# Optimization experiments

Hardware: AMD Instinct MI355X
Metric: run time of the kernel (lower is better)

## Reference

```python
import jax, jax.numpy as jnp
import numpy as np

B, H, W, C, N, P = 4, 200, 176, 256, 16384, 65536
EPS = 1e-3  # BatchNorm eps from the torch module


def _bn(x, g, b, axes):
    # training-mode batch norm (batch statistics), matching nn.BatchNorm forward
    m = x.mean(axes, keepdims=True)
    v = x.var(axes, keepdims=True)
    return (x - m) * jax.lax.rsqrt(v + EPS) * g + b


def setup_inputs() -> dict:
    key = jax.random.key(0)
    ks = jax.random.split(key, 16)
    s = 0.05
    d = {}
    d['feats'] = jax.random.normal(ks[0], (B, C, N), jnp.float32)
    d['cb'] = jax.random.randint(ks[1], (P,), 0, B, dtype=jnp.int32)
    d['cy'] = jax.random.randint(ks[2], (P,), 0, H, dtype=jnp.int32)
    d['cx'] = jax.random.randint(ks[3], (P,), 0, W, dtype=jnp.int32)
    # SH head: Linear(256,256,nb)+BN+ReLU, Linear(256,256,nb)+BN+ReLU, Linear(256,9,b)
    d['sh_w1'] = jax.random.normal(ks[4], (C, 256), jnp.float32) * s
    d['sh_g1'] = jnp.ones((256,), jnp.float32); d['sh_b1'] = jnp.zeros((256,), jnp.float32)
    d['sh_w2'] = jax.random.normal(ks[5], (256, 256), jnp.float32) * s
    d['sh_g2'] = jnp.ones((256,), jnp.float32); d['sh_b2'] = jnp.zeros((256,), jnp.float32)
    d['sh_w3'] = jax.random.normal(ks[6], (256, 9), jnp.float32) * s
    d['sh_bias3'] = jnp.zeros((9,), jnp.float32)
    # Gaus head: Linear(256,256,nb)+BN+ReLU, Linear(256,128,nb)+BN+ReLU, Linear(128,1,b)+sigmoid
    d['g_w1'] = jax.random.normal(ks[7], (C, 256), jnp.float32) * s
    d['g_g1'] = jnp.ones((256,), jnp.float32); d['g_b1'] = jnp.zeros((256,), jnp.float32)
    d['g_w2'] = jax.random.normal(ks[8], (256, 128), jnp.float32) * s
    d['g_g2'] = jnp.ones((128,), jnp.float32); d['g_b2'] = jnp.zeros((128,), jnp.float32)
    d['g_w3'] = jax.random.normal(ks[9], (128, 1), jnp.float32) * s
    d['g_bias3'] = jnp.zeros((1,), jnp.float32)
    # conv_out: 3x3 SparseConv2d no-bias + BN + ReLU ; shared_conv: 3x3 SubMConv2d bias + BN + ReLU
    d['cw1'] = jax.random.normal(ks[10], (3, 3, C, C), jnp.float32) * s
    d['c1_g'] = jnp.ones((C,), jnp.float32); d['c1_b'] = jnp.zeros((C,), jnp.float32)
    d['cw2'] = jax.random.normal(ks[11], (3, 3, C, C), jnp.float32) * s
    d['c2_bias'] = jnp.zeros((C,), jnp.float32)
    d['c2_g'] = jnp.ones((C,), jnp.float32); d['c2_b'] = jnp.zeros((C,), jnp.float32)
    return d


def reference(feats, cb, cy, cx, sh_w1, sh_g1, sh_b1, sh_w2, sh_g2, sh_b2, sh_w3, sh_bias3,
              g_w1, g_g1, g_b1, g_w2, g_g2, g_b2, g_w3, g_bias3,
              cw1, c1_g, c1_b, cw2, c2_bias, c2_g, c2_b):
    # [B,C,N] -> [B*N, C] point-wise features
    pw = feats.transpose(0, 2, 1).reshape(-1, C)
    # pool_feature_in_same_voxel: mean of point features sharing a voxel
    vid = cb * (H * W) + cy * W + cx  # [P] linear voxel id over dense BEV grid
    S = B * H * W
    sums = jax.ops.segment_sum(pw, vid, num_segments=S)            # [S, C]
    cnt = jax.ops.segment_sum(jnp.ones((P,), pw.dtype), vid, num_segments=S)
    pooled = sums / jnp.maximum(cnt, 1.0)[:, None]                 # [S, C]
    # SH head
    h = jax.nn.relu(_bn(pooled @ sh_w1, sh_g1, sh_b1, 0))
    h = jax.nn.relu(_bn(h @ sh_w2, sh_g2, sh_b2, 0))
    pred_sh = h @ sh_w3 + sh_bias3                                 # [S, 9]
    # Gaussian head
    g = jax.nn.relu(_bn(pooled @ g_w1, g_g1, g_b1, 0))
    g = jax.nn.relu(_bn(g @ g_w2, g_g2, g_b2, 0))
    pred_gaus = jax.nn.sigmoid(g @ g_w3 + g_bias3)                 # [S, 1]
    # get_sparse_voxel_feature3: SH (DC term) + gaussian modulated voxel features
    sp = pooled * pred_gaus * pred_sh[:, :1]                       # [S, C]
    x = sp.reshape(B, H, W, C)                                      # dense BEV sparse-tensor equivalent
    dn = ('NHWC', 'HWIO', 'NHWC')
    x = jax.lax.conv_general_dilated(x, cw1, (1, 1), 'SAME', dimension_numbers=dn)
    x = jax.nn.relu(_bn(x, c1_g, c1_b, (0, 1, 2)))
    x = jax.lax.conv_general_dilated(x, cw2, (1, 1), 'SAME', dimension_numbers=dn) + c2_bias
    x = jax.nn.relu(_bn(x, c2_g, c2_b, (0, 1, 2)))
    return x
```

## Files before the change

kernel.cpp:

```cpp
#include <hip/hip_runtime.h>
#include <hip/hip_bf16.h>
#include <cstdint>
#include <cstddef>

#define B_DIM 4
#define H_DIM 200
#define W_DIM 176
#define CCH 256
#define NPP 16384
#define NPTS 65536
#define HW 35200
#define S_TOT 140800
#define EPS 1e-3f
#define INV_S (1.0f/140800.0f)

typedef unsigned short ushort_t;
typedef __attribute__((ext_vector_type(8))) short bf16x8;
typedef __attribute__((ext_vector_type(4))) float f32x4;

__device__ __forceinline__ ushort_t f2bf(float f) {
    __hip_bfloat16 h = __float2bfloat16(f);
    return *(ushort_t*)&h;
}
__device__ __forceinline__ float bf2f(ushort_t u) {
    __hip_bfloat16 h = *(__hip_bfloat16*)&u;
    return __bfloat162float(h);
}

__device__ __forceinline__ void async16(const void* g, void* l) {
    __builtin_amdgcn_global_load_lds(
        (const __attribute__((address_space(1))) unsigned int*)g,
        (__attribute__((address_space(3))) unsigned int*)l,
        16, 0, 0);
}

__device__ __forceinline__ void wait_vmcnt0()  { asm volatile("s_waitcnt vmcnt(0)" ::: "memory"); }
__device__ __forceinline__ void wait_vmcnt4()  { asm volatile("s_waitcnt vmcnt(4)" ::: "memory"); }
__device__ __forceinline__ void wait_vmcnt8()  { asm volatile("s_waitcnt vmcnt(8)" ::: "memory"); }
__device__ __forceinline__ void wait_vmcnt10() { asm volatile("s_waitcnt vmcnt(10)" ::: "memory"); }
__device__ __forceinline__ void wait_lgkm0()   { asm volatile("s_waitcnt lgkmcnt(0)" ::: "memory"); }
__device__ __forceinline__ void memfence_compiler() { asm volatile("" ::: "memory"); }

__device__ __forceinline__ bf16x8 bnrelu8(bf16x8 a, const float* __restrict__ sc,
                                          const float* __restrict__ sh) {
    bf16x8 r;
#pragma unroll
    for (int e = 0; e < 8; ++e) {
        float f = bf2f((ushort_t)a[e]);
        r[e] = (short)f2bf(fmaxf(0.f, f * sc[e] + sh[e]));
    }
    return r;
}

__device__ __forceinline__ int xcd_virt(int fid, int n) {
    int q = n >> 3, r = n & 7;
    int xcd = fid & 7, idx = fid >> 3;
    int base = (xcd < r) ? xcd * (q + 1) : r * (q + 1) + (xcd - r) * q;
    return base + idx;
}

__global__ __launch_bounds__(256) void k_transpose(
    const float* __restrict__ feats, ushort_t* __restrict__ FT)
{
    __shared__ float lds[64][65];
    const int b  = blockIdx.z;
    const int c0 = blockIdx.y * 64;
    const int n0 = blockIdx.x * 64;
    const int tid = threadIdx.x;
#pragma unroll
    for (int i = 0; i < 16; ++i) {
        int idx = i * 256 + tid;
        int cr = idx >> 6, nc = idx & 63;
        lds[cr][nc] = feats[((size_t)b * 256 + c0 + cr) * NPP + n0 + nc];
    }
    __syncthreads();
#pragma unroll
    for (int i = 0; i < 16; ++i) {
        int idx = i * 256 + tid;
        int nr = idx >> 6, cc = idx & 63;
        FT[((size_t)b * NPP + n0 + nr) * CCH + c0 + cc] = f2bf(lds[cc][nr]);
    }
}

__global__ __launch_bounds__(256) void k_buildidx(
    const int* __restrict__ cb, const int* __restrict__ cy,
    const int* __restrict__ cx, int* __restrict__ cnt,
    int* __restrict__ pslot, int* __restrict__ vid)
{
    int p = blockIdx.x * 256 + threadIdx.x;
    int v = cb[p] * HW + cy[p] * W_DIM + cx[p];
    vid[p] = v;
    int r = atomicAdd(&cnt[v], 1);
    if (r < 8) pslot[v * 8 + r] = p;
}

__global__ __launch_bounds__(256) void k_poolgather(
    const ushort_t* __restrict__ FT, const int* __restrict__ cnt,
    const int* __restrict__ pslot, const int* __restrict__ vid,
    ushort_t* __restrict__ Pb)
{
    const int wave = threadIdx.x >> 6;
    const int lane = threadIdx.x & 63;
    const int v = blockIdx.x * 4 + wave;
    const int c = cnt[v];
    float a0 = 0.f, a1 = 0.f, a2 = 0.f, a3 = 0.f;
    if (c <= 8) {
        for (int k = 0; k < c; ++k) {
            int p = pslot[v * 8 + k];
            ushort4 r = ((const ushort4*)(FT + (size_t)p * CCH))[lane];
            a0 += bf2f(r.x); a1 += bf2f(r.y); a2 += bf2f(r.z); a3 += bf2f(r.w);
        }
    } else {
        for (int p = 0; p < NPTS; ++p)
            if (vid[p] == v) {
                ushort4 r = ((const ushort4*)(FT + (size_t)p * CCH))[lane];
                a0 += bf2f(r.x); a1 += bf2f(r.y); a2 += bf2f(r.z); a3 += bf2f(r.w);
            }
    }
    float inv = c ? 1.f / (float)c : 0.f;
    ushort4 o;
    o.x = f2bf(a0 * inv); o.y = f2bf(a1 * inv);
    o.z = f2bf(a2 * inv); o.w = f2bf(a3 * inv);
    ((ushort4*)(Pb + (size_t)v * CCH))[lane] = o;
}

__global__ __launch_bounds__(256) void k_gemmma(
    const ushort_t* __restrict__ X, const ushort_t* __restrict__ Wt,
    ushort_t* __restrict__ Y1, ushort_t* __restrict__ Y2, int ldY,
    int bnh, int nblocks,
    float* __restrict__ acc0, float* __restrict__ acc1, int sqoff)
{
    __shared__ ushort_t Asm[2][128 * 64];
    __shared__ ushort_t Bsm[2][128 * 64];
    const int tid  = threadIdx.x;
    const int w    = tid >> 6;
    const int lane = tid & 63;
    const int virt = xcd_virt(blockIdx.x, nblocks);
    const int pi   = virt / bnh;
    const int bn   = (virt % bnh) * 128;
    const int bm   = pi * 128;
    const int wr   = (w >> 1) * 64;
    const int wc   = (w & 1) * 64;

    size_t aoff[4]; size_t boff[4];
#pragma unroll
    for (int j = 0; j < 4; ++j) {
        int row  = 32 * j + 8 * w + (lane >> 3);
        int qlog = (lane & 7) ^ (row & 7);
        aoff[j] = (size_t)(bm + row) * 256 + qlog * 8;
        boff[j] = (size_t)(bn + row) * 256 + qlog * 8;
    }
    const int lo = (w * 8) * 64;

#pragma unroll
    for (int j = 0; j < 4; ++j) async16(X + aoff[j], &Asm[0][(j * 32) * 64 + lo]);
#pragma unroll
    for (int j = 0; j < 4; ++j) async16(Wt + boff[j], &Bsm[0][(j * 32) * 64 + lo]);

    f32x4 acc[4][4] = {};
    for (int kc = 0; kc < 4; ++kc) {
        if (kc < 3) {
#pragma unroll
            for (int j = 0; j < 4; ++j)
                async16(X + aoff[j] + (kc + 1) * 64, &Asm[(kc + 1) & 1][(j * 32) * 64 + lo]);
#pragma unroll
            for (int j = 0; j < 4; ++j)
                async16(Wt + boff[j] + (kc + 1) * 64, &Bsm[(kc + 1) & 1][(j * 32) * 64 + lo]);
            wait_vmcnt8();
        } else {
            wait_vmcnt0();
        }
        __builtin_amdgcn_s_barrier();
        const ushort_t* Ac = Asm[kc & 1];
        const ushort_t* Bc = Bsm[kc & 1];
        __builtin_amdgcn_s_setprio(1);
#pragma unroll
        for (int ks = 0; ks < 2; ++ks) {
            const int q = ks * 4 + (lane >> 4);
            bf16x8 af[4], bfr[4];
#pragma unroll
            for (int i = 0; i < 4; ++i) {
                int ra = wr + i * 16 + (lane & 15);
                af[i] = *(const bf16x8*)&Ac[ra * 64 + ((q ^ (ra & 7)) * 8)];
            }
#pragma unroll
            for (int jn = 0; jn < 4; ++jn) {
                int rn = wc + jn * 16 + (lane & 15);
                bfr[jn] = *(const bf16x8*)&Bc[rn * 64 + ((q ^ (rn & 7)) * 8)];
            }
#pragma unroll
            for (int i = 0; i < 4; ++i)
#pragma unroll
                for (int jn = 0; jn < 4; ++jn)
                    acc[i][jn] = __builtin_amdgcn_mfma_f32_16x16x32_bf16(
                        af[i], bfr[jn], acc[i][jn], 0, 0, 0);
        }
        __builtin_amdgcn_s_setprio(0);
        memfence_compiler();
        __builtin_amdgcn_s_barrier();
    }
    __syncthreads();

    const int crow0 = bm + wr + (lane >> 4) * 4;
    const int ccol0 = bn + wc + (lane & 15);
    float ls[4] = {}, lq[4] = {};
#pragma unroll
    for (int i = 0; i < 4; ++i)
#pragma unroll
        for (int jn = 0; jn < 4; ++jn) {
            int col = ccol0 + jn * 16;
#pragma unroll
            for (int r = 0; r < 4; ++r) {
                float v = acc[i][jn][r];
                ls[jn] += v; lq[jn] += v * v;
                size_t row = (size_t)(crow0 + i * 16 + r);
                if (col < 256) Y1[row * ldY + col] = f2bf(v);
                else           Y2[row * ldY + col - 256] = f2bf(v);
            }
        }
#pragma unroll
    for (int jn = 0; jn < 4; ++jn) {
        ls[jn] += __shfl_xor(ls[jn], 16, 64); ls[jn] += __shfl_xor(ls[jn], 32, 64);
        lq[jn] += __shfl_xor(lq[jn], 16, 64); lq[jn] += __shfl_xor(lq[jn], 32, 64);
    }
    float* red = (float*)&Asm[0][0];
    if (lane < 16) {
#pragma unroll
        for (int jn = 0; jn < 4; ++jn) {
            red[((w * 16 + lane) * 4 + jn) * 2 + 0] = ls[jn];
            red[((w * 16 + lane) * 4 + jn) * 2 + 1] = lq[jn];
        }
    }
    __syncthreads();
    if (tid < 256) {
        int colhalf = tid & 127, isq = tid >> 7;
        int pair = colhalf >> 6, within = colhalf & 63;
        int l16 = within & 15, jn = within >> 4;
        int w0 = pair ? 1 : 0, w1 = pair ? 3 : 2;
        float s = red[((w0 * 16 + l16) * 4 + jn) * 2 + isq]
                + red[((w1 * 16 + l16) * 4 + jn) * 2 + isq];
        int colg = bn + colhalf;
        float* t = (colg < 256) ? acc0 : acc1;
        atomicAdd(&t[(colg & 255) + isq * sqoff], s);
    }
}

__global__ __launch_bounds__(256) void k_gemmma_bn2(
    const ushort_t* __restrict__ X1, const float* __restrict__ a1In,
    const float* __restrict__ g1, const float* __restrict__ b1,
    const ushort_t* __restrict__ W1, ushort_t* __restrict__ Y1o,
    float* __restrict__ a1Out,
    const ushort_t* __restrict__ X2, const float* __restrict__ a2In,
    const float* __restrict__ g2, const float* __restrict__ b2,
    const ushort_t* __restrict__ W2, ushort_t* __restrict__ Y2o,
    float* __restrict__ a2Out)
{
    const bool sh = blockIdx.x < 2200;
    const ushort_t* X   = sh ? X1 : X2;
    const float* accIn  = sh ? a1In : a2In;
    const float* gIn    = sh ? g1 : g2;
    const float* bIn    = sh ? b1 : b2;
    const ushort_t* Wt  = sh ? W1 : W2;
    ushort_t* Y         = sh ? Y1o : Y2o;
    float* accOut       = sh ? a1Out : a2Out;
    const int ldY       = sh ? 256 : 128;
    const int bnh       = sh ? 2 : 1;
    const int fid       = sh ? blockIdx.x : blockIdx.x - 2200;
    const int nblocks   = sh ? 2200 : 1100;
    const int sqoff     = ldY;

    __shared__ ushort_t Asm[2][128 * 64];
    __shared__ ushort_t Bsm[2][128 * 64];
    __shared__ float parS[512];
    const int tid  = threadIdx.x;
    const int w    = tid >> 6;
    const int lane = tid & 63;
    {
        float m = accIn[tid] * INV_S;
        float v = accIn[256 + tid] * INV_S - m * m;
        float sc = gIn[tid] * rsqrtf(v + EPS);
        parS[tid] = sc;
        parS[256 + tid] = bIn[tid] - m * sc;
    }
    __syncthreads();

    const int virt = xcd_virt(fid, nblocks);
    const int pi   = virt / bnh;
    const int bn   = (virt % bnh) * 128;
    const int bm   = pi * 128;
    const int wr   = (w >> 1) * 64;
    const int wc   = (w & 1) * 64;

    const int qlog = (lane & 7) ^ ((8 * w + (lane >> 3)) & 7);
    size_t aoff[4]; size_t boff[4]; int arow[4];
#pragma unroll
    for (int j = 0; j < 4; ++j) {
        int row  = 32 * j + 8 * w + (lane >> 3);
        arow[j] = row;
        aoff[j] = (size_t)(bm + row) * 256 + qlog * 8;
        boff[j] = (size_t)(bn + row) * 256 + qlog * 8;
    }
    const int lo = (w * 8) * 64;
    const int lsub = (lane & 7) * 8;

    bf16x8 ar[2][4];
#pragma unroll
    for (int j = 0; j < 4; ++j) async16(Wt + boff[j], &Bsm[0][(j * 32) * 64 + lo]);
#pragma unroll
    for (int j = 0; j < 4; ++j) ar[0][j] = *(const bf16x8*)(X + aoff[j]);
    {
        const int cb = qlog * 8;
#pragma unroll
        for (int j = 0; j < 4; ++j)
            *(bf16x8*)&Asm[0][arow[j] * 64 + lsub] =
                bnrelu8(ar[0][j], parS + cb, parS + 256 + cb);
    }
    wait_lgkm0();

    f32x4 acc[4][4] = {};
#pragma unroll
    for (int kc = 0; kc < 4; ++kc) {
        if (kc < 3) {
#pragma unroll
            for (int j = 0; j < 4; ++j)
                async16(Wt + boff[j] + (kc + 1) * 64, &Bsm[(kc + 1) & 1][(j * 32) * 64 + lo]);
#pragma unroll
            for (int j = 0; j < 4; ++j)
                ar[(kc + 1) & 1][j] = *(const bf16x8*)(X + aoff[j] + (kc + 1) * 64);
            wait_vmcnt8();
        } else {
            wait_vmcnt0();
        }
        __builtin_amdgcn_s_barrier();
        const ushort_t* Ac = Asm[kc & 1];
        const ushort_t* Bc = Bsm[kc & 1];
        __builtin_amdgcn_s_setprio(1);
#pragma unroll
        for (int ks = 0; ks < 2; ++ks) {
            const int q = ks * 4 + (lane >> 4);
            bf16x8 af[4], bfr[4];
#pragma unroll
            for (int i = 0; i < 4; ++i) {
                int ra = wr + i * 16 + (lane & 15);
                af[i] = *(const bf16x8*)&Ac[ra * 64 + ((q ^ (ra & 7)) * 8)];
            }
#pragma unroll
            for (int jn = 0; jn < 4; ++jn) {
                int rn = wc + jn * 16 + (lane & 15);
                bfr[jn] = *(const bf16x8*)&Bc[rn * 64 + ((q ^ (rn & 7)) * 8)];
            }
#pragma unroll
            for (int i = 0; i < 4; ++i)
#pragma unroll
                for (int jn = 0; jn < 4; ++jn)
                    acc[i][jn] = __builtin_amdgcn_mfma_f32_16x16x32_bf16(
                        af[i], bfr[jn], acc[i][jn], 0, 0, 0);
        }
        __builtin_amdgcn_s_setprio(0);
        if (kc < 3) {
            const int cb = (kc + 1) * 64 + qlog * 8;
#pragma unroll
            for (int j = 0; j < 4; ++j)
                *(bf16x8*)&Asm[(kc + 1) & 1][arow[j] * 64 + lsub] =
                    bnrelu8(ar[(kc + 1) & 1][j], parS + cb, parS + 256 + cb);
            wait_lgkm0();
        }
        memfence_compiler();
        __builtin_amdgcn_s_barrier();
    }
    __syncthreads();

    const int crow0 = bm + wr + (lane >> 4) * 4;
    const int ccol0 = bn + wc + (lane & 15);
    float ls[4] = {}, lq[4] = {};
#pragma unroll
    for (int i = 0; i < 4; ++i)
#pragma unroll
        for (int jn = 0; jn < 4; ++jn) {
            int col = ccol0 + jn * 16;
#pragma unroll
            for (int r = 0; r < 4; ++r) {
                float v = acc[i][jn][r];
                ls[jn] += v; lq[jn] += v * v;
                Y[(size_t)(crow0 + i * 16 + r) * ldY + col] = f2bf(v);
            }
        }
#pragma unroll
    for (int jn = 0; jn < 4; ++jn) {
        ls[jn] += __shfl_xor(ls[jn], 16, 64); ls[jn] += __shfl_xor(ls[jn], 32, 64);
        lq[jn] += __shfl_xor(lq[jn], 16, 64); lq[jn] += __shfl_xor(lq[jn], 32, 64);
    }
    float* red = (float*)&Asm[0][0];
    if (lane < 16) {
#pragma unroll
        for (int jn = 0; jn < 4; ++jn) {
            red[((w * 16 + lane) * 4 + jn) * 2 + 0] = ls[jn];
            red[((w * 16 + lane) * 4 + jn) * 2 + 1] = lq[jn];
        }
    }
    __syncthreads();
    if (tid < 256) {
        int colhalf = tid & 127, isq = tid >> 7;
        int pair = colhalf >> 6, within = colhalf & 63;
        int l16 = within & 15, jn = within >> 4;
        int w0 = pair ? 1 : 0, w1 = pair ? 3 : 2;
        float s = red[((w0 * 16 + l16) * 4 + jn) * 2 + isq]
                + red[((w1 * 16 + l16) * 4 + jn) * 2 + isq];
        atomicAdd(&accOut[(bn + colhalf) + isq * sqoff], s);
    }
}

__global__ __launch_bounds__(256) void k_convmma(
    const ushort_t* __restrict__ X, const ushort_t* __restrict__ Wt,
    ushort_t* __restrict__ Yb, const float* __restrict__ bias,
    const ushort_t* __restrict__ zp, float* __restrict__ accp)
{
    __shared__ ushort_t Asm[2][192 * 64];
    __shared__ ushort_t Bsm[2][128 * 64];
    const int tid  = threadIdx.x;
    const int w    = tid >> 6;
    const int lane = tid & 63;
    const int virt = xcd_virt(blockIdx.x, 2200);
    const int pi   = virt >> 1;
    const int bn   = (virt & 1) * 128;
    const int b    = pi / 275;
    const int rem  = pi % 275;
    const int th   = rem / 11, tw = rem % 11;
    const int y0   = th * 8 - 1, x0 = tw * 16 - 1;
    const int hb   = (w >> 1) * 4;
    const int wc   = (w & 1) * 64;

    const int qlog = (lane & 7) ^ (lane >> 3);
    const ushort_t* asrc[6];
#pragma unroll
    for (int j = 0; j < 6; ++j) {
        int hr = j * 32 + w * 8 + (lane >> 3);
        int ph = hr / 18, pw = hr % 18;
        int y = y0 + ph, x = x0 + pw;
        bool ok = (hr < 180) && ((unsigned)y < (unsigned)H_DIM) &&
                  ((unsigned)x < (unsigned)W_DIM);
        asrc[j] = ok ? X + ((size_t)b * HW + (size_t)y * W_DIM + x) * 256 + qlog * 8
                     : zp + (lane & 7) * 8;
    }
    const ushort_t* bsrc = Wt + (size_t)(bn + w * 8 + (lane >> 3)) * 256 + qlog * 8;
    const int lo = (w * 8) * 64;

#pragma unroll
    for (int j = 0; j < 6; ++j)
        async16(asrc[j], &Asm[0][(j * 32) * 64 + lo]);
#pragma unroll
    for (int j = 0; j < 4; ++j)
        async16(bsrc + (size_t)j * 8192, &Bsm[0][(j * 32) * 64 + lo]);

    f32x4 acc[4][4] = {};
    for (int kc = 0; kc < 4; ++kc) {
        const ushort_t* acur = Asm[kc & 1];
#pragma unroll
        for (int pos = 0; pos < 9; ++pos) {
            const ushort_t* bcur = Bsm[(kc + pos) & 1];
            ushort_t* bnxt = (ushort_t*)Bsm[(kc + pos + 1) & 1];
            if (pos == 0) {
                if (kc < 3) {
#pragma unroll
                    for (int j = 0; j < 6; ++j)
                        async16(asrc[j] + (kc + 1) * 64,
                                &Asm[(kc + 1) & 1][(j * 32) * 64 + lo]);
#pragma unroll
                    for (int j = 0; j < 4; ++j)
                        async16(bsrc + (size_t)65536 + kc * 64 + j * 8192,
                                bnxt + (j * 32) * 64 + lo);
                    wait_vmcnt10();
                } else {
#pragma unroll
                    for (int j = 0; j < 4; ++j)
                        async16(bsrc + (size_t)65536 + kc * 64 + j * 8192,
                                bnxt + (j * 32) * 64 + lo);
                    wait_vmcnt4();
                }
            } else if (pos < 8) {
#pragma unroll
                for (int j = 0; j < 4; ++j)
                    async16(bsrc + (size_t)(pos + 1) * 65536 + kc * 64 + j * 8192,
                            bnxt + (j * 32) * 64 + lo);
                wait_vmcnt4();
            } else if (kc < 3) {
#pragma unroll
                for (int j = 0; j < 4; ++j)
                    async16(bsrc + (size_t)(kc + 1) * 64 + j * 8192,
                            bnxt + (j * 32) * 64 + lo);
                wait_vmcnt4();
            } else {
                wait_vmcnt0();
            }
            __builtin_amdgcn_s_barrier();
            const int dy = pos / 3 - 1, dx = pos % 3 - 1;
            __builtin_amdgcn_s_setprio(1);
#pragma unroll
            for (int ks = 0; ks < 2; ++ks) {
                const int q = ks * 4 + (lane >> 4);
                bf16x8 af[4], bfr[4];
#pragma unroll
                for (int i = 0; i < 4; ++i) {
                    int ri = (hb + i + 1 + dy) * 18 + 1 + dx + (lane & 15);
                    af[i] = *(const bf16x8*)&acur[ri * 64 + ((q ^ (ri & 7)) * 8)];
                }
#pragma unroll
                for (int jn = 0; jn < 4; ++jn) {
                    int rn = wc + jn * 16 + (lane & 15);
                    bfr[jn] = *(const bf16x8*)&bcur[rn * 64 + ((q ^ (rn & 7)) * 8)];
                }
#pragma unroll
                for (int i = 0; i < 4; ++i)
#pragma unroll
                    for (int jn = 0; jn < 4; ++jn)
                        acc[i][jn] = __builtin_amdgcn_mfma_f32_16x16x32_bf16(
                            af[i], bfr[jn], acc[i][jn], 0, 0, 0);
            }
            __builtin_amdgcn_s_setprio(0);
            memfence_compiler();
            __builtin_amdgcn_s_barrier();
        }
    }
    __syncthreads();

    const size_t sbase = (size_t)b * HW + (size_t)(th * 8) * W_DIM + tw * 16;
    const int colb = bn + wc + (lane & 15);
    const int wsub = (lane >> 4) * 4;
    float ls[4] = {}, lq[4] = {};
#pragma unroll
    for (int i = 0; i < 4; ++i) {
        int h = hb + i;
#pragma unroll
        for (int jn = 0; jn < 4; ++jn) {
            int col = colb + jn * 16;
            float bb = bias ? bias[col] : 0.f;
#pragma unroll
            for (int r = 0; r < 4; ++r) {
                size_t s = sbase + (size_t)h * W_DIM + wsub + r;
                float v = acc[i][jn][r] + bb;
                ls[jn] += v; lq[jn] += v * v;
                Yb[s * 256 + col] = f2bf(v);
            }
        }
    }
#pragma unroll
    for (int jn = 0; jn < 4; ++jn) {
        ls[jn] += __shfl_xor(ls[jn], 16, 64); ls[jn] += __shfl_xor(ls[jn], 32, 64);
        lq[jn] += __shfl_xor(lq[jn], 16, 64); lq[jn] += __shfl_xor(lq[jn], 32, 64);
    }
    float* red = (float*)&Asm[0][0];
    if (lane < 16) {
#pragma unroll
        for (int jn = 0; jn < 4; ++jn) {
            red[((w * 16 + lane) * 4 + jn) * 2 + 0] = ls[jn];
            red[((w * 16 + lane) * 4 + jn) * 2 + 1] = lq[jn];
        }
    }
    __syncthreads();
    if (tid < 256) {
        int colhalf = tid & 127, isq = tid >> 7;
        int pair = colhalf >> 6, within = colhalf & 63;
        int l16 = within & 15, jn = within >> 4;
        int w0 = pair ? 1 : 0, w1 = pair ? 3 : 2;
        float s = red[((w0 * 16 + l16) * 4 + jn) * 2 + isq]
                + red[((w1 * 16 + l16) * 4 + jn) * 2 + isq];
        atomicAdd(&accp[(bn + colhalf) + isq * 256], s);
    }
}

__global__ __launch_bounds__(256) void k_convmma_bn(
    const ushort_t* __restrict__ X, const float* __restrict__ par,
    const ushort_t* __restrict__ Wt,
    ushort_t* __restrict__ Yb, const float* __restrict__ bias,
    const ushort_t* __restrict__ zp, float* __restrict__ accp)
{
    __shared__ ushort_t Asm[2][192 * 64];
    __shared__ ushort_t Bsm[2][128 * 64];
    const int tid  = threadIdx.x;
    const int w    = tid >> 6;
    const int lane = tid & 63;
    const int virt = xcd_virt(blockIdx.x, 2200);
    const int pi   = virt >> 1;
    const int bn   = (virt & 1) * 128;
    const int b    = pi / 275;
    const int rem  = pi % 275;
    const int th   = rem / 11, tw = rem % 11;
    const int y0   = th * 8 - 1, x0 = tw * 16 - 1;
    const int hb   = (w >> 1) * 4;
    const int wc   = (w & 1) * 64;

    const int qlog = (lane & 7) ^ (lane >> 3);
    const ushort_t* asrc[6];
    bool okj[6];
    int arow[6];
#pragma unroll
    for (int j = 0; j < 6; ++j) {
        int hr = j * 32 + w * 8 + (lane >> 3);
        arow[j] = hr;
        int ph = hr / 18, pw = hr % 18;
        int y = y0 + ph, x = x0 + pw;
        okj[j] = (hr < 180) && ((unsigned)y < (unsigned)H_DIM) &&
                 ((unsigned)x < (unsigned)W_DIM);
        asrc[j] = okj[j] ? X + ((size_t)b * HW + (size_t)y * W_DIM + x) * 256 + qlog * 8
                         : zp + (lane & 7) * 8;
    }
    const ushort_t* bsrc = Wt + (size_t)(bn + w * 8 + (lane >> 3)) * 256 + qlog * 8;
    const int lo = (w * 8) * 64;
    const int lsub = (lane & 7) * 8;
    const bf16x8 zv = 0;

    bf16x8 areg[6];
#pragma unroll
    for (int j = 0; j < 6; ++j) areg[j] = *(const bf16x8*)(asrc[j]);
#pragma unroll
    for (int j = 0; j < 4; ++j)
        async16(bsrc + (size_t)j * 8192, &Bsm[0][(j * 32) * 64 + lo]);
    {
        const int cb = qlog * 8;
#pragma unroll
        for (int j = 0; j < 6; ++j)
            *(bf16x8*)&Asm[0][arow[j] * 64 + lsub] =
                okj[j] ? bnrelu8(areg[j], par + cb, par + 256 + cb) : zv;
    }
    wait_lgkm0();

    f32x4 acc[4][4] = {};
#pragma unroll
    for (int kc = 0; kc < 4; ++kc) {
        const ushort_t* acur = Asm[kc & 1];
#pragma unroll
        for (int pos = 0; pos < 9; ++pos) {
            const ushort_t* bcur = Bsm[(kc + pos) & 1];
            ushort_t* bnxt = (ushort_t*)Bsm[(kc + pos + 1) & 1];
            if (pos < 8) {
#pragma unroll
                for (int j = 0; j < 4; ++j)
                    async16(bsrc + (size_t)(pos + 1) * 65536 + kc * 64 + j * 8192,
                            bnxt + (j * 32) * 64 + lo);
            } else if (kc < 3) {
#pragma unroll
                for (int j = 0; j < 4; ++j)
                    async16(bsrc + (size_t)(kc + 1) * 64 + j * 8192,
                            bnxt + (j * 32) * 64 + lo);
            }
            if (pos == 5 && kc < 3) {
#pragma unroll
                for (int j = 0; j < 6; ++j)
                    areg[j] = *(const bf16x8*)(asrc[j] + (kc + 1) * 64);
            }
            if (kc == 3 && pos == 8)      wait_vmcnt0();
            else if (pos == 6 && kc < 3)  wait_vmcnt10();
            else                          wait_vmcnt4();
            __builtin_amdgcn_s_barrier();
            const int dy = pos / 3 - 1, dx = pos % 3 - 1;
            __builtin_amdgcn_s_setprio(1);
#pragma unroll
            for (int ks = 0; ks < 2; ++ks) {
                const int q = ks * 4 + (lane >> 4);
                bf16x8 af[4], bfr[4];
#pragma unroll
                for (int i = 0; i < 4; ++i) {
                    int ri = (hb + i + 1 + dy) * 18 + 1 + dx + (lane & 15);
                    af[i] = *(const bf16x8*)&acur[ri * 64 + ((q ^ (ri & 7)) * 8)];
                }
#pragma unroll
                for (int jn = 0; jn < 4; ++jn) {
                    int rn = wc + jn * 16 + (lane & 15);
                    bfr[jn] = *(const bf16x8*)&bcur[rn * 64 + ((q ^ (rn & 7)) * 8)];
                }
#pragma unroll
                for (int i = 0; i < 4; ++i)
#pragma unroll
                    for (int jn = 0; jn < 4; ++jn)
                        acc[i][jn] = __builtin_amdgcn_mfma_f32_16x16x32_bf16(
                            af[i], bfr[jn], acc[i][jn], 0, 0, 0);
            }
            __builtin_amdgcn_s_setprio(0);
            if (pos == 8 && kc < 3) {
                const int cb = (kc + 1) * 64 + qlog * 8;
#pragma unroll
                for (int j = 0; j < 6; ++j)
                    *(bf16x8*)&Asm[(kc + 1) & 1][arow[j] * 64 + lsub] =
                        okj[j] ? bnrelu8(areg[j], par + cb, par + 256 + cb) : zv;
                wait_lgkm0();
            }
            memfence_compiler();
            __builtin_amdgcn_s_barrier();
        }
    }
    __syncthreads();

    const size_t sbase = (size_t)b * HW + (size_t)(th * 8) * W_DIM + tw * 16;
    const int colb = bn + wc + (lane & 15);
    const int wsub = (lane >> 4) * 4;
    float ls[4] = {}, lq[4] = {};
#pragma unroll
    for (int i = 0; i < 4; ++i) {
        int h = hb + i;
#pragma unroll
        for (int jn = 0; jn < 4; ++jn) {
            int col = colb + jn * 16;
            float bb = bias ? bias[col] : 0.f;
#pragma unroll
            for (int r = 0; r < 4; ++r) {
                size_t s = sbase + (size_t)h * W_DIM + wsub + r;
                float v = acc[i][jn][r] + bb;
                ls[jn] += v; lq[jn] += v * v;
                Yb[s * 256 + col] = f2bf(v);
            }
        }
    }
#pragma unroll
    for (int jn = 0; jn < 4; ++jn) {
        ls[jn] += __shfl_xor(ls[jn], 16, 64); ls[jn] += __shfl_xor(ls[jn], 32, 64);
        lq[jn] += __shfl_xor(lq[jn], 16, 64); lq[jn] += __shfl_xor(lq[jn], 32, 64);
    }
    float* red = (float*)&Asm[0][0];
    if (lane < 16) {
#pragma unroll
        for (int jn = 0; jn < 4; ++jn) {
            red[((w * 16 + lane) * 4 + jn) * 2 + 0] = ls[jn];
            red[((w * 16 + lane) * 4 + jn) * 2 + 1] = lq[jn];
        }
    }
    __syncthreads();
    if (tid < 256) {
        int colhalf = tid & 127, isq = tid >> 7;
        int pair = colhalf >> 6, within = colhalf & 63;
        int l16 = within & 15, jn = within >> 4;
        int w0 = pair ? 1 : 0, w1 = pair ? 3 : 2;
        float s = red[((w0 * 16 + l16) * 4 + jn) * 2 + isq]
                + red[((w1 * 16 + l16) * 4 + jn) * 2 + isq];
        atomicAdd(&accp[(bn + colhalf) + isq * 256], s);
    }
}

__global__ __launch_bounds__(256) void k_castw(
    const float* __restrict__ Wc, ushort_t* __restrict__ Wt, int CO)
{
    int pc = blockIdx.x;
    int co = pc % CO, pos = pc / CO, ci = threadIdx.x;
    Wt[(size_t)pc * 256 + ci] = f2bf(Wc[((size_t)pos * 256 + ci) * CO + co]);
}

__global__ void k_bnparams(const float* __restrict__ acc,
                           const float* __restrict__ g,
                           const float* __restrict__ b,
                           float* __restrict__ par, int ncols)
{
    int c = threadIdx.x;
    if (c >= ncols) return;
    float m = acc[c] * INV_S;
    float v = acc[ncols + c] * INV_S - m * m;
    float sc = g[c] * rsqrtf(v + EPS);
    par[c] = sc;
    par[ncols + c] = b[c] - m * sc;
}

__global__ __launch_bounds__(256) void k_headfin(
    const ushort_t* __restrict__ B2, const ushort_t* __restrict__ B3,
    const float* __restrict__ acc1, const float* __restrict__ shg2,
    const float* __restrict__ shb2,
    const float* __restrict__ acc3, const float* __restrict__ gg2,
    const float* __restrict__ gb2,
    const float* __restrict__ shw3, const float* __restrict__ shb3,
    const float* __restrict__ gw3, const float* __restrict__ gb3,
    const ushort_t* __restrict__ Pb, ushort_t* __restrict__ Xb)
{
    __shared__ float parA[512], parB[256];
    const int t = threadIdx.x;
    {
        float m = acc1[t] * INV_S;
        float v = acc1[256 + t] * INV_S - m * m;
        float sc = shg2[t] * rsqrtf(v + EPS);
        parA[t] = sc; parA[256 + t] = shb2[t] - m * sc;
    }
    if (t < 128) {
        float m = acc3[t] * INV_S;
        float v = acc3[128 + t] * INV_S - m * m;
        float sc = gg2[t] * rsqrtf(v + EPS);
        parB[t] = sc; parB[128 + t] = gb2[t] - m * sc;
    }
    __syncthreads();

    const int wave = t >> 6;
    const int lane = t & 63;
    const int s = blockIdx.x * 4 + wave;
    const ushort_t* b2 = B2 + (size_t)s * 256;
    const ushort_t* b3 = B3 + (size_t)s * 128;
    float d1 = 0.f, d2 = 0.f;
    {
        ushort4 u = ((const ushort4*)b2)[lane];
        int c = lane * 4;
        float v0 = fmaxf(0.f, bf2f(u.x) * parA[c + 0] + parA[256 + c + 0]);
        float v1 = fmaxf(0.f, bf2f(u.y) * parA[c + 1] + parA[256 + c + 1]);
        float v2 = fmaxf(0.f, bf2f(u.z) * parA[c + 2] + parA[256 + c + 2]);
        float v3 = fmaxf(0.f, bf2f(u.w) * parA[c + 3] + parA[256 + c + 3]);
        d1 = v0 * shw3[(c + 0) * 9] + v1 * shw3[(c + 1) * 9]
           + v2 * shw3[(c + 2) * 9] + v3 * shw3[(c + 3) * 9];
    }
    {
        ushort2 u = ((const ushort2*)b3)[lane];
        int c = lane * 2;
        float v0 = fmaxf(0.f, bf2f(u.x) * parB[c + 0] + parB[128 + c + 0]);
        float v1 = fmaxf(0.f, bf2f(u.y) * parB[c + 1] + parB[128 + c + 1]);
        d2 = v0 * gw3[c + 0] + v1 * gw3[c + 1];
    }
#pragma unroll
    for (int off = 32; off > 0; off >>= 1) {
        d1 += __shfl_down(d1, off, 64);
        d2 += __shfl_down(d2, off, 64);
    }
    d1 = __shfl(d1, 0, 64);
    d2 = __shfl(d2, 0, 64);
    float shdc = d1 + shb3[0];
    float gaus = 1.f / (1.f + expf(-(d2 + gb3[0])));
    float factor = shdc * gaus;
    ushort4 pv = ((const ushort4*)(Pb + (size_t)s * 256))[lane];
    ushort4 o;
    o.x = f2bf(bf2f(pv.x) * factor);
    o.y = f2bf(bf2f(pv.y) * factor);
    o.z = f2bf(bf2f(pv.z) * factor);
    o.w = f2bf(bf2f(pv.w) * factor);
    ((ushort4*)(Xb + (size_t)s * 256))[lane] = o;
}

__global__ __launch_bounds__(256) void k_bnrelu_f32out(
    const ushort_t* __restrict__ Y, const float* __restrict__ acc5,
    const float* __restrict__ g, const float* __restrict__ b,
    float* __restrict__ out)
{
    __shared__ float par[512];
    const int t = threadIdx.x;
    {
        float m = acc5[t] * INV_S;
        float v = acc5[256 + t] * INV_S - m * m;
        float sc = g[t] * rsqrtf(v + EPS);
        par[t] = sc; par[256 + t] = b[t] - m * sc;
    }
    __syncthreads();
    size_t q = (size_t)blockIdx.x * 256 + t;
    int c = (int)(q & 63) * 4;
    ushort4 u = ((const ushort4*)Y)[q];
    float4 v;
    v.x = fmaxf(0.f, bf2f(u.x) * par[c + 0] + par[256 + c + 0]);
    v.y = fmaxf(0.f, bf2f(u.y) * par[c + 1] + par[256 + c + 1]);
    v.z = fmaxf(0.f, bf2f(u.z) * par[c + 2] + par[256 + c + 2]);
    v.w = fmaxf(0.f, bf2f(u.w) * par[c + 3] + par[256 + c + 3]);
    ((float4*)out)[q] = v;
}

extern "C" void kernel_launch(void* const* d_in, const int* in_sizes, int n_in,
                              void* d_out, int out_size, void* d_ws, size_t ws_size,
                              hipStream_t stream)
{
    (void)in_sizes; (void)n_in; (void)out_size; (void)ws_size;
    const float* feats   = (const float*)d_in[0];
    const int*   cb      = (const int*)d_in[1];
    const int*   cy      = (const int*)d_in[2];
    const int*   cx      = (const int*)d_in[3];
    const float* sh_w1   = (const float*)d_in[4];
    const float* sh_g1   = (const float*)d_in[5];
    const float* sh_b1   = (const float*)d_in[6];
    const float* sh_w2   = (const float*)d_in[7];
    const float* sh_g2   = (const float*)d_in[8];
    const float* sh_b2   = (const float*)d_in[9];
    const float* sh_w3   = (const float*)d_in[10];
    const float* sh_bias3= (const float*)d_in[11];
    const float* g_w1    = (const float*)d_in[12];
    const float* g_g1    = (const float*)d_in[13];
    const float* g_b1    = (const float*)d_in[14];
    const float* g_w2    = (const float*)d_in[15];
    const float* g_g2    = (const float*)d_in[16];
    const float* g_b2    = (const float*)d_in[17];
    const float* g_w3    = (const float*)d_in[18];
    const float* g_bias3 = (const float*)d_in[19];
    const float* cw1     = (const float*)d_in[20];
    const float* c1_g    = (const float*)d_in[21];
    const float* c1_b    = (const float*)d_in[22];
    const float* cw2     = (const float*)d_in[23];
    const float* c2_bias = (const float*)d_in[24];
    const float* c2_g    = (const float*)d_in[25];
    const float* c2_b    = (const float*)d_in[26];

    float* out = (float*)d_out;
    float* ws  = (float*)d_ws;
    ushort_t* Pb   = (ushort_t*)(ws);
    ushort_t* Bsh  = (ushort_t*)(ws + 18022400);
    ushort_t* Bg   = (ushort_t*)(ws + 36044800);
    ushort_t* Cb   = (ushort_t*)(ws + 54067200);
    ushort_t* FT   = (ushort_t*)(ws + 54067200);
    ushort_t* Db   = (ushort_t*)(ws + 72089600);
    int*      CNTi = (int*)(ws + 72089600);
    int*      PSL  = CNTi + S_TOT;
    int*      VID  = PSL + S_TOT * 8;
    ushort_t* Eb   = Pb;
    ushort_t* WCAT = (ushort_t*)(ws + 81100800);
    ushort_t* WS2  = WCAT + 131072;
    ushort_t* WG2  = WS2 + 65536;
    ushort_t* WT1  = WG2 + 32768;
    ushort_t* WT2  = WT1 + 589824;
    ushort_t* ZP   = WT2 + 589824;
    float*    ACC  = (float*)(ZP + 2048);
    float*    PAR  = ACC + 6 * 512;

    hipMemsetAsync(CNTi, 0, (size_t)S_TOT * 4, stream);
    hipMemsetAsync(ACC, 0, 6 * 512 * 4, stream);
    hipMemsetAsync(ZP, 0, 4096, stream);

    k_castw<<<256, 256, 0, stream>>>(sh_w1, WCAT, 256);
    k_castw<<<256, 256, 0, stream>>>(g_w1, WCAT + 65536, 256);
    k_castw<<<256, 256, 0, stream>>>(sh_w2, WS2, 256);
    k_castw<<<128, 256, 0, stream>>>(g_w2, WG2, 128);
    k_castw<<<9 * 256, 256, 0, stream>>>(cw1, WT1, 256);
    k_castw<<<9 * 256, 256, 0, stream>>>(cw2, WT2, 256);

    k_transpose<<<dim3(256, 4, 4), 256, 0, stream>>>(feats, FT);
    k_buildidx<<<NPTS / 256, 256, 0, stream>>>(cb, cy, cx, CNTi, PSL, VID);
    k_poolgather<<<S_TOT / 4, 256, 0, stream>>>(FT, CNTi, PSL, VID, Pb);

    k_gemmma<<<4400, 256, 0, stream>>>(Pb, WCAT, Bsh, Bg, 256, 4, 4400,
                                       ACC + 0 * 512, ACC + 2 * 512, 256);
    k_gemmma_bn2<<<3300, 256, 0, stream>>>(
        Bsh, ACC + 0 * 512, sh_g1, sh_b1, WS2, Cb, ACC + 1 * 512,
        Bg,  ACC + 2 * 512, g_g1,  g_b1,  WG2, Db, ACC + 3 * 512);
    k_headfin<<<S_TOT / 4, 256, 0, stream>>>(Cb, Db,
                                             ACC + 1 * 512, sh_g2, sh_b2,
                                             ACC + 3 * 512, g_g2, g_b2,
                                             sh_w3, sh_bias3, g_w3, g_bias3,
                                             Pb, Bsh);
    k_convmma<<<2200, 256, 0, stream>>>(Bsh, WT1, Eb, nullptr, ZP, ACC + 4 * 512);
    k_bnparams<<<1, 256, 0, stream>>>(ACC + 4 * 512, c1_g, c1_b, PAR, 256);
    k_convmma_bn<<<2200, 256, 0, stream>>>(Eb, PAR, WT2, Bsh, c2_bias, ZP,
                                           ACC + 5 * 512);
    k_bnrelu_f32out<<<35200, 256, 0, stream>>>(Bsh, ACC + 5 * 512, c2_g, c2_b, out);
}
```

Measured before the change: 730.4 us.

## Fuse per-voxel scaling into first conv A-tile load and merge weight casts

The head-finish kernel now writes only a per-voxel scalar factor instead of rewriting the full scaled feature tensor. The first conv kernel loads the pooled features into registers, multiplies them by that factor and stores them to LDS, so one full [S,256] bf16 write and read pass is avoided. Because the A tile now goes through registers instead of async copies, its prefetch is reissued mid-loop with adjusted waits. The six weight-cast launches are merged into a single kernel, and the buffers are reassigned so conv outputs avoid aliasing.

```diff
diff --git a/kernel.cpp b/kernel.cpp
--- a/kernel.cpp
+++ b/kernel.cpp
@@ -49,6 +49,14 @@
         float f = bf2f((ushort_t)a[e]);
         r[e] = (short)f2bf(fmaxf(0.f, f * sc[e] + sh[e]));
     }
+    return r;
+}
+
+__device__ __forceinline__ bf16x8 mul8(bf16x8 a, float f) {
+    bf16x8 r;
+#pragma unroll
+    for (int e = 0; e < 8; ++e)
+        r[e] = (short)f2bf(bf2f((ushort_t)a[e]) * f);
     return r;
 }
 
@@ -410,8 +418,9 @@
     }
 }
 
-__global__ __launch_bounds__(256) void k_convmma(
-    const ushort_t* __restrict__ X, const ushort_t* __restrict__ Wt,
+__global__ __launch_bounds__(256) void k_convmma_fac(
+    const ushort_t* __restrict__ X, const float* __restrict__ FAC,
+    const ushort_t* __restrict__ Wt,
     ushort_t* __restrict__ Yb, const float* __restrict__ bias,
     const ushort_t* __restrict__ zp, float* __restrict__ accp)
 {
@@ -432,66 +441,67 @@
 
     const int qlog = (lane & 7) ^ (lane >> 3);
     const ushort_t* asrc[6];
+    bool okj[6];
+    int arow[6];
+    float fj[6];
 #pragma unroll
     for (int j = 0; j < 6; ++j) {
         int hr = j * 32 + w * 8 + (lane >> 3);
+        arow[j] = hr;
         int ph = hr / 18, pw = hr % 18;
         int y = y0 + ph, x = x0 + pw;
-        bool ok = (hr < 180) && ((unsigned)y < (unsigned)H_DIM) &&
-                  ((unsigned)x < (unsigned)W_DIM);
-        asrc[j] = ok ? X + ((size_t)b * HW + (size_t)y * W_DIM + x) * 256 + qlog * 8
-                     : zp + (lane & 7) * 8;
+        okj[j] = (hr < 180) && ((unsigned)y < (unsigned)H_DIM) &&
+                 ((unsigned)x < (unsigned)W_DIM);
+        size_t s = (size_t)b * HW + (size_t)y * W_DIM + x;
+        asrc[j] = okj[j] ? X + s * 256 + qlog * 8 : zp + (lane & 7) * 8;
+        fj[j] = okj[j] ? FAC[s] : 0.f;
     }
     const ushort_t* bsrc = Wt + (size_t)(bn + w * 8 + (lane >> 3)) * 256 + qlog * 8;
     const int lo = (w * 8) * 64;
-
-#pragma unroll
-    for (int j = 0; j < 6; ++j)
-        async16(asrc[j], &Asm[0][(j * 32) * 64 + lo]);
+    const int lsub = (lane & 7) * 8;
+    const bf16x8 zv = 0;
+
+    bf16x8 areg[6];
+#pragma unroll
+    for (int j = 0; j < 6; ++j) areg[j] = *(const bf16x8*)(asrc[j]);
 #pragma unroll
     for (int j = 0; j < 4; ++j)
         async16(bsrc + (size_t)j * 8192, &Bsm[0][(j * 32) * 64 + lo]);
+    {
+#pragma unroll
+        for (int j = 0; j < 6; ++j)
+            *(bf16x8*)&Asm[0][arow[j] * 64 + lsub] =
+                okj[j] ? mul8(areg[j], fj[j]) : zv;
+    }
+    wait_lgkm0();
 
     f32x4 acc[4][4] = {};
+#pragma unroll
     for (int kc = 0; kc < 4; ++kc) {
         const ushort_t* acur = Asm[kc & 1];
 #pragma unroll
         for (int pos = 0; pos < 9; ++pos) {
             const ushort_t* bcur = Bsm[(kc + pos) & 1];
             ushort_t* bnxt = (ushort_t*)Bsm[(kc + pos + 1) & 1];
-            if (pos == 0) {
-                if (kc < 3) {
-#pragma unroll
-                    for (int j = 0; j < 6; ++j)
-                        async16(asrc[j] + (kc + 1) * 64,
-                                &Asm[(kc + 1) & 1][(j * 32) * 64 + lo]);
-#pragma unroll
-                    for (int j = 0; j < 4; ++j)
-                        async16(bsrc + (size_t)65536 + kc * 64 + j * 8192,
-                                bnxt + (j * 32) * 64 + lo);
-                    wait_vmcnt10();
-                } else {
-#pragma unroll
-                    for (int j = 0; j < 4; ++j)
-                        async16(bsrc + (size_t)65536 + kc * 64 + j * 8192,
-                                bnxt + (j * 32) * 64 + lo);
-                    wait_vmcnt4();
-                }
-            } else if (pos < 8) {
+            if (pos < 8) {
 #pragma unroll
                 for (int j = 0; j < 4; ++j)
                     async16(bsrc + (size_t)(pos + 1) * 65536 + kc * 64 + j * 8192,
                             bnxt + (j * 32) * 64 + lo);
-                wait_vmcnt4();
             } else if (kc < 3) {
 #pragma unroll
                 for (int j = 0; j < 4; ++j)
                     async16(bsrc + (size_t)(kc + 1) * 64 + j * 8192,
                             bnxt + (j * 32) * 64 + lo);
-                wait_vmcnt4();
-            } else {
-                wait_vmcnt0();
-            }
+            }
+            if (pos == 5 && kc < 3) {
+#pragma unroll
+                for (int j = 0; j < 6; ++j)
+                    areg[j] = *(const bf16x8*)(asrc[j] + (kc + 1) * 64);
+            }
+            if (kc == 3 && pos == 8)      wait_vmcnt0();
+            else if (pos == 6 && kc < 3)  wait_vmcnt10();
+            else                          wait_vmcnt4();
             __builtin_amdgcn_s_barrier();
             const int dy = pos / 3 - 1, dx = pos % 3 - 1;
             __builtin_amdgcn_s_setprio(1);
@@ -517,6 +527,13 @@
                             af[i], bfr[jn], acc[i][jn], 0, 0, 0);
             }
             __builtin_amdgcn_s_setprio(0);
+            if (pos == 8 && kc < 3) {
+#pragma unroll
+                for (int j = 0; j < 6; ++j)
+                    *(bf16x8*)&Asm[(kc + 1) & 1][arow[j] * 64 + lsub] =
+                        okj[j] ? mul8(areg[j], fj[j]) : zv;
+                wait_lgkm0();
+            }
             memfence_compiler();
             __builtin_amdgcn_s_barrier();
         }
@@ -735,12 +752,24 @@
     }
 }
 
-__global__ __launch_bounds__(256) void k_castw(
-    const float* __restrict__ Wc, ushort_t* __restrict__ Wt, int CO)
-{
-    int pc = blockIdx.x;
-    int co = pc % CO, pos = pc / CO, ci = threadIdx.x;
-    Wt[(size_t)pc * 256 + ci] = f2bf(Wc[((size_t)pos * 256 + ci) * CO + co]);
+__global__ __launch_bounds__(256) void k_castw_all(
+    const float* __restrict__ cw1, const float* __restrict__ cw2,
+    const float* __restrict__ shw1, const float* __restrict__ gw1,
+    const float* __restrict__ shw2, const float* __restrict__ gw2,
+    ushort_t* __restrict__ WT1, ushort_t* __restrict__ WT2,
+    ushort_t* __restrict__ WCAT, ushort_t* __restrict__ WS2,
+    ushort_t* __restrict__ WG2)
+{
+    const int bid = blockIdx.x, ci = threadIdx.x;
+    const float* src; ushort_t* dst; int CO, pc;
+    if (bid < 2304)      { src = cw1;  dst = WT1;          CO = 256; pc = bid; }
+    else if (bid < 4608) { src = cw2;  dst = WT2;          CO = 256; pc = bid - 2304; }
+    else if (bid < 4864) { src = shw1; dst = WCAT;         CO = 256; pc = bid - 4608; }
+    else if (bid < 5120) { src = gw1;  dst = WCAT + 65536; CO = 256; pc = bid - 4864; }
+    else if (bid < 5376) { src = shw2; dst = WS2;          CO = 256; pc = bid - 5120; }
+    else                 { src = gw2;  dst = WG2;          CO = 128; pc = bid - 5376; }
+    int co = pc % CO, pos = pc / CO;
+    dst[(size_t)pc * 256 + ci] = f2bf(src[((size_t)pos * 256 + ci) * CO + co]);
 }
 
 __global__ void k_bnparams(const float* __restrict__ acc,
@@ -757,7 +786,7 @@
     par[ncols + c] = b[c] - m * sc;
 }
 
-__global__ __launch_bounds__(256) void k_headfin(
+__global__ __launch_bounds__(256) void k_headfin_fac(
     const ushort_t* __restrict__ B2, const ushort_t* __restrict__ B3,
     const float* __restrict__ acc1, const float* __restrict__ shg2,
     const float* __restrict__ shb2,
@@ -765,7 +794,7 @@
     const float* __restrict__ gb2,
     const float* __restrict__ shw3, const float* __restrict__ shb3,
     const float* __restrict__ gw3, const float* __restrict__ gb3,
-    const ushort_t* __restrict__ Pb, ushort_t* __restrict__ Xb)
+    float* __restrict__ FAC)
 {
     __shared__ float parA[512], parB[256];
     const int t = threadIdx.x;
@@ -811,18 +840,11 @@
         d1 += __shfl_down(d1, off, 64);
         d2 += __shfl_down(d2, off, 64);
     }
-    d1 = __shfl(d1, 0, 64);
-    d2 = __shfl(d2, 0, 64);
-    float shdc = d1 + shb3[0];
-    float gaus = 1.f / (1.f + expf(-(d2 + gb3[0])));
-    float factor = shdc * gaus;
-    ushort4 pv = ((const ushort4*)(Pb + (size_t)s * 256))[lane];
-    ushort4 o;
-    o.x = f2bf(bf2f(pv.x) * factor);
-    o.y = f2bf(bf2f(pv.y) * factor);
-    o.z = f2bf(bf2f(pv.z) * factor);
-    o.w = f2bf(bf2f(pv.w) * factor);
-    ((ushort4*)(Xb + (size_t)s * 256))[lane] = o;
+    if (lane == 0) {
+        float shdc = d1 + shb3[0];
+        float gaus = 1.f / (1.f + expf(-(d2 + gb3[0])));
+        FAC[s] = shdc * gaus;
+    }
 }
 
 __global__ __launch_bounds__(256) void k_bnrelu_f32out(
@@ -894,7 +916,6 @@
     int*      CNTi = (int*)(ws + 72089600);
     int*      PSL  = CNTi + S_TOT;
     int*      VID  = PSL + S_TOT * 8;
-    ushort_t* Eb   = Pb;
     ushort_t* WCAT = (ushort_t*)(ws + 81100800);
     ushort_t* WS2  = WCAT + 131072;
     ushort_t* WG2  = WS2 + 65536;
@@ -903,17 +924,14 @@
     ushort_t* ZP   = WT2 + 589824;
     float*    ACC  = (float*)(ZP + 2048);
     float*    PAR  = ACC + 6 * 512;
+    float*    FAC  = PAR + 512;
 
     hipMemsetAsync(CNTi, 0, (size_t)S_TOT * 4, stream);
     hipMemsetAsync(ACC, 0, 6 * 512 * 4, stream);
     hipMemsetAsync(ZP, 0, 4096, stream);
 
-    k_castw<<<256, 256, 0, stream>>>(sh_w1, WCAT, 256);
-    k_castw<<<256, 256, 0, stream>>>(g_w1, WCAT + 65536, 256);
-    k_castw<<<256, 256, 0, stream>>>(sh_w2, WS2, 256);
-    k_castw<<<128, 256, 0, stream>>>(g_w2, WG2, 128);
-    k_castw<<<9 * 256, 256, 0, stream>>>(cw1, WT1, 256);
-    k_castw<<<9 * 256, 256, 0, stream>>>(cw2, WT2, 256);
+    k_castw_all<<<5504, 256, 0, stream>>>(cw1, cw2, sh_w1, g_w1, sh_w2, g_w2,
+                                          WT1, WT2, WCAT, WS2, WG2);
 
     k_transpose<<<dim3(256, 4, 4), 256, 0, stream>>>(feats, FT);
     k_buildidx<<<NPTS / 256, 256, 0, stream>>>(cb, cy, cx, CNTi, PSL, VID);
@@ -924,14 +942,15 @@
     k_gemmma_bn2<<<3300, 256, 0, stream>>>(
         Bsh, ACC + 0 * 512, sh_g1, sh_b1, WS2, Cb, ACC + 1 * 512,
         Bg,  ACC + 2 * 512, g_g1,  g_b1,  WG2, Db, ACC + 3 * 512);
-    k_headfin<<<S_TOT / 4, 256, 0, stream>>>(Cb, Db,
-                                             ACC + 1 * 512, sh_g2, sh_b2,
-                                             ACC + 3 * 512, g_g2, g_b2,
-                                             sh_w3, sh_bias3, g_w3, g_bias3,
-                                             Pb, Bsh);
-    k_convmma<<<2200, 256, 0, stream>>>(Bsh, WT1, Eb, nullptr, ZP, ACC + 4 * 512);
+    k_headfin_fac<<<S_TOT / 4, 256, 0, stream>>>(Cb, Db,
+                                                 ACC + 1 * 512, sh_g2, sh_b2,
+                                                 ACC + 3 * 512, g_g2, g_b2,
+                                                 sh_w3, sh_bias3, g_w3, g_bias3,
+                                                 FAC);
+    k_convmma_fac<<<2200, 256, 0, stream>>>(Pb, FAC, WT1, Bsh, nullptr, ZP,
+                                            ACC + 4 * 512);
     k_bnparams<<<1, 256, 0, stream>>>(ACC + 4 * 512, c1_g, c1_b, PAR, 256);
-    k_convmma_bn<<<2200, 256, 0, stream>>>(Eb, PAR, WT2, Bsh, c2_bias, ZP,
+    k_convmma_bn<<<2200, 256, 0, stream>>>(Bsh, PAR, WT2, Cb, c2_bias, ZP,
                                            ACC + 5 * 512);
-    k_bnrelu_f32out<<<35200, 256, 0, stream>>>(Bsh, ACC + 5 * 512, c2_g, c2_b, out);
-}
+    k_bnrelu_f32out<<<35200, 256, 0, stream>>>(Cb, ACC + 5 * 512, c2_g, c2_b, out);
+}
```

Measured after the change: 779.2 us. 6.7% more time.
